# Performance work log

Measured on AMD Instinct MI355X. Metric: run time of the kernel, lower is better.

Reference implementation:

```python
import jax, jax.numpy as jnp
import numpy as np

N = 50000
NEG_SLOPE = 0.2


def add_self_loops(edge_index, n):
    loop = jnp.arange(n, dtype=edge_index.dtype)
    return jnp.concatenate([edge_index, jnp.stack([loop, loop])], axis=1)


def gatv2_conv(x, edge_index, Wl, bl, Wr, br, att, bias):
    """PyG GATv2Conv (share_weights=False, concat=True, add_self_loops applied by caller).
    x: [N, Fin]; edge_index: [2, E] with row0=src(j), row1=dst(i); att: [H, D].
    Returns (out [N, H*D], alpha [E, H])."""
    src, dst = edge_index[0], edge_index[1]
    H, D = att.shape
    n = x.shape[0]
    xl = (x @ Wl + bl).reshape(n, H, D)   # source-side transform
    xr = (x @ Wr + br).reshape(n, H, D)   # target-side transform
    e = jax.nn.leaky_relu(xl[src] + xr[dst], NEG_SLOPE)        # [E, H, D]
    logit = jnp.einsum('ehd,hd->eh', e, att)                    # [E, H]
    # segment softmax over edges grouped by target node
    lmax = jax.ops.segment_max(logit, dst, num_segments=n)      # [N, H]
    ex = jnp.exp(logit - lmax[dst])
    denom = jax.ops.segment_sum(ex, dst, num_segments=n)
    alpha = ex / denom[dst]                                     # [E, H]
    out = jax.ops.segment_sum(alpha[:, :, None] * xl[src], dst, num_segments=n)  # [N, H, D]
    return out.reshape(n, H * D) + bias, alpha


def setup_inputs() -> dict:
    key = jax.random.key(0)
    ks = jax.random.split(key, 16)
    E = 400000
    x = jax.random.normal(ks[0], (N, 23), dtype=jnp.float32)
    edge_index = jax.random.randint(ks[1], (2, E), 0, N, dtype=jnp.int64)
    H1, D1 = 8, 64
    F1 = H1 * D1  # 512
    s = 0.1
    return {
        'x': x,
        'edge_index': edge_index,
        'Wl1': jax.random.normal(ks[2], (23, F1), dtype=jnp.float32) * s,
        'bl1': jnp.zeros((F1,), jnp.float32),
        'Wr1': jax.random.normal(ks[3], (23, F1), dtype=jnp.float32) * s,
        'br1': jnp.zeros((F1,), jnp.float32),
        'att1': jax.random.normal(ks[4], (H1, D1), dtype=jnp.float32) * s,
        'bias1': jnp.zeros((F1,), jnp.float32),
        'Wl2': jax.random.normal(ks[5], (F1, 1), dtype=jnp.float32) * s,
        'bl2': jnp.zeros((1,), jnp.float32),
        'Wr2': jax.random.normal(ks[6], (F1, 1), dtype=jnp.float32) * s,
        'br2': jnp.zeros((1,), jnp.float32),
        'att2': jax.random.normal(ks[7], (1, 1), dtype=jnp.float32) * s,
        'bias2': jnp.zeros((1,), jnp.float32),
    }


def reference(x, edge_index, Wl1, bl1, Wr1, br1, att1, bias1,
              Wl2, bl2, Wr2, br2, att2, bias2):
    ei = add_self_loops(edge_index, N)
    h, _ = gatv2_conv(x, ei, Wl1, bl1, Wr1, br1, att1, bias1)
    h = jax.nn.relu(h)
    h, alpha = gatv2_conv(h, ei, Wl2, bl2, Wr2, br2, att2, bias2)
    return h, alpha
```

## Files before the change

### kernel.cpp

```cpp
#include <hip/hip_runtime.h>
#include <math.h>

#define NN 50000
#define E0 400000
#define EE 450000
#define FF 512
#define G1 2048
#define NPB 25
#define EPB 220
#define WAVES_TOTAL (G1 * 4)
#define MAXD 64
#define LOG2E 1.44269504f

typedef _Float16 h2 __attribute__((ext_vector_type(2)));

__device__ __forceinline__ h2 uas_h2(unsigned u) { union { unsigned u; h2 h; } c; c.u = u; return c.h; }
__device__ __forceinline__ unsigned h2as_u(h2 h) { union { unsigned u; h2 h; } c; c.h = h; return c.u; }
__device__ __forceinline__ float leaky(float v) { return fmaxf(v, 0.2f * v); }

__global__ __launch_bounds__(256) void k_predeg(
    const float* __restrict__ x,
    const float* __restrict__ Wl1, const float* __restrict__ bl1,
    const float* __restrict__ Wr1, const float* __restrict__ br1,
    const int* __restrict__ ei,
    unsigned* __restrict__ xlh, unsigned* __restrict__ xrh,
    int* __restrict__ cnt, uint2* __restrict__ slots)
{
    __shared__ float sx[NPB * 23];
    int b = blockIdx.x, t = threadIdx.x;

    {
        int e0 = b * EPB;
        int e1 = e0 + EPB; if (e1 > EE) e1 = EE;
        for (int e = e0 + t; e < e1; e += 256) {
            int src, dst;
            if (e < E0) { src = ei[e]; dst = ei[E0 + e]; }
            else        { src = e - E0; dst = src; }
            int p = atomicAdd(&cnt[dst], 1);
            if (p < MAXD) slots[(size_t)dst * MAXD + p] = make_uint2((unsigned)src, (unsigned)e);
        }
    }

    int i0 = b * NPB;
    int i1 = i0 + NPB; if (i1 > NN) i1 = NN;
    int nnod = i1 - i0;
    int nf = nnod * 23;
    for (int k = t; k < nf; k += 256) sx[k] = x[(size_t)i0 * 23 + k];
    __syncthreads();

    int c0 = 2 * t, c1 = 2 * t + 1;
    {
        float w0[23], w1[23];
#pragma unroll
        for (int r = 0; r < 23; r++) { w0[r] = Wl1[r * FF + c0]; w1[r] = Wl1[r * FF + c1]; }
        float bb0 = bl1[c0], bb1 = bl1[c1];
        for (int n = 0; n < nnod; n++) {
            float a0 = bb0, a1 = bb1;
#pragma unroll
            for (int r = 0; r < 23; r++) { float xv = sx[n * 23 + r]; a0 += xv * w0[r]; a1 += xv * w1[r]; }
            h2 hh = { (_Float16)a0, (_Float16)a1 };
            xlh[(size_t)(i0 + n) * 256 + t] = h2as_u(hh);
        }
    }
    {
        float w0[23], w1[23];
#pragma unroll
        for (int r = 0; r < 23; r++) { w0[r] = Wr1[r * FF + c0]; w1[r] = Wr1[r * FF + c1]; }
        float bb0 = br1[c0], bb1 = br1[c1];
        for (int n = 0; n < nnod; n++) {
            float a0 = bb0, a1 = bb1;
#pragma unroll
            for (int r = 0; r < 23; r++) { float xv = sx[n * 23 + r]; a0 += xv * w0[r]; a1 += xv * w1[r]; }
            h2 hh = { (_Float16)a0, (_Float16)a1 };
            xrh[(size_t)(i0 + n) * 256 + t] = h2as_u(hh);
        }
    }
}

__global__ __launch_bounds__(256) void k_layer1(
    const uint4* __restrict__ xlh, const uint4* __restrict__ xrh,
    const float* __restrict__ att, const float* __restrict__ bias1,
    const float* __restrict__ Wl2, const float* __restrict__ bl2,
    const float* __restrict__ Wr2, const float* __restrict__ br2,
    const int* __restrict__ cnt, const uint2* __restrict__ slots,
    float* __restrict__ xl2, float* __restrict__ xr2)
{
    int t = threadIdx.x;
    int l = t & 63;
    int wid = blockIdx.x * 4 + (t >> 6);

    float4 atA = ((const float4*)att)[2 * l];
    float4 atB = ((const float4*)att)[2 * l + 1];
    h2 a6_0 = { (_Float16)(0.6f * LOG2E * atA.x), (_Float16)(0.6f * LOG2E * atA.y) };
    h2 a6_1 = { (_Float16)(0.6f * LOG2E * atA.z), (_Float16)(0.6f * LOG2E * atA.w) };
    h2 a6_2 = { (_Float16)(0.6f * LOG2E * atB.x), (_Float16)(0.6f * LOG2E * atB.y) };
    h2 a6_3 = { (_Float16)(0.6f * LOG2E * atB.z), (_Float16)(0.6f * LOG2E * atB.w) };
    h2 a4_0 = { (_Float16)(0.4f * LOG2E * atA.x), (_Float16)(0.4f * LOG2E * atA.y) };
    h2 a4_1 = { (_Float16)(0.4f * LOG2E * atA.z), (_Float16)(0.4f * LOG2E * atA.w) };
    h2 a4_2 = { (_Float16)(0.4f * LOG2E * atB.x), (_Float16)(0.4f * LOG2E * atB.y) };
    h2 a4_3 = { (_Float16)(0.4f * LOG2E * atB.z), (_Float16)(0.4f * LOG2E * atB.w) };
    float bl2v = bl2[0], br2v = br2[0];

    for (int i = wid; i < NN; i += WAVES_TOTAL) {
        uint4 xq = xrh[(size_t)i * 64 + l];
        h2 q0 = uas_h2(xq.x), q1 = uas_h2(xq.y), q2 = uas_h2(xq.z), q3 = uas_h2(xq.w);

        float s = 0.f;
        h2 A0 = { 0, 0 }, A1 = { 0, 0 }, A2 = { 0, 0 }, A3 = { 0, 0 };

        int dg = cnt[i]; if (dg > MAXD) dg = MAXD;
        int myj = (l < dg) ? (int)slots[(size_t)i * MAXD + l].x : 0;

        int j0 = __builtin_amdgcn_readlane(myj, 0);
        uint4 r0 = xlh[(size_t)j0 * 64 + l];
        uint4 r1 = r0;
        if (dg > 1) r1 = xlh[(size_t)__builtin_amdgcn_readlane(myj, 1) * 64 + l];

        for (int p = 0; p < dg; p++) {
            uint4 rn = r0;
            if (p + 2 < dg)
                rn = xlh[(size_t)__builtin_amdgcn_readlane(myj, p + 2) * 64 + l];

            h2 p0 = uas_h2(r0.x), p1 = uas_h2(r0.y), p2 = uas_h2(r0.z), p3 = uas_h2(r0.w);
            h2 t0 = p0 + q0, t1 = p1 + q1, t2 = p2 + q2, t3 = p3 + q3;
            h2 b0 = uas_h2(h2as_u(t0) & 0x7fff7fffu);
            h2 b1 = uas_h2(h2as_u(t1) & 0x7fff7fffu);
            h2 b2 = uas_h2(h2as_u(t2) & 0x7fff7fffu);
            h2 b3 = uas_h2(h2as_u(t3) & 0x7fff7fffu);
            float part = 0.f;
            part = __builtin_amdgcn_fdot2(a6_0, t0, part, false);
            part = __builtin_amdgcn_fdot2(a4_0, b0, part, false);
            part = __builtin_amdgcn_fdot2(a6_1, t1, part, false);
            part = __builtin_amdgcn_fdot2(a4_1, b1, part, false);
            part = __builtin_amdgcn_fdot2(a6_2, t2, part, false);
            part = __builtin_amdgcn_fdot2(a4_2, b2, part, false);
            part = __builtin_amdgcn_fdot2(a6_3, t3, part, false);
            part = __builtin_amdgcn_fdot2(a4_3, b3, part, false);
            part += __shfl_xor(part, 1, 64);
            part += __shfl_xor(part, 2, 64);
            part += __shfl_xor(part, 4, 64);
            float wv = exp2f(part);
            s += wv;
            _Float16 wh = (_Float16)wv;
            h2 w2 = { wh, wh };
            A0 += w2 * p0;
            A1 += w2 * p1;
            A2 += w2 * p2;
            A3 += w2 * p3;
            r0 = r1; r1 = rn;
        }

        float inv = 1.f / s;
        float4 bA = ((const float4*)bias1)[2 * l];
        float4 bB = ((const float4*)bias1)[2 * l + 1];
        float h0 = fmaxf(fmaf((float)A0[0], inv, bA.x), 0.f);
        float h1 = fmaxf(fmaf((float)A0[1], inv, bA.y), 0.f);
        float h2v = fmaxf(fmaf((float)A1[0], inv, bA.z), 0.f);
        float h3 = fmaxf(fmaf((float)A1[1], inv, bA.w), 0.f);
        float h4 = fmaxf(fmaf((float)A2[0], inv, bB.x), 0.f);
        float h5 = fmaxf(fmaf((float)A2[1], inv, bB.y), 0.f);
        float h6 = fmaxf(fmaf((float)A3[0], inv, bB.z), 0.f);
        float h7 = fmaxf(fmaf((float)A3[1], inv, bB.w), 0.f);

        float4 wlA = ((const float4*)Wl2)[2 * l];
        float4 wlB = ((const float4*)Wl2)[2 * l + 1];
        float4 wrA = ((const float4*)Wr2)[2 * l];
        float4 wrB = ((const float4*)Wr2)[2 * l + 1];
        float pl = h0 * wlA.x + h1 * wlA.y + h2v * wlA.z + h3 * wlA.w
                 + h4 * wlB.x + h5 * wlB.y + h6 * wlB.z + h7 * wlB.w;
        float pr = h0 * wrA.x + h1 * wrA.y + h2v * wrA.z + h3 * wrA.w
                 + h4 * wrB.x + h5 * wrB.y + h6 * wrB.z + h7 * wrB.w;
#pragma unroll
        for (int o = 32; o > 0; o >>= 1) {
            pl += __shfl_xor(pl, o, 64);
            pr += __shfl_xor(pr, o, 64);
        }
        if (l == 0) {
            xl2[i] = pl + bl2v;
            xr2[i] = pr + br2v;
        }
    }
}

__global__ void k_layer2(const float* __restrict__ xl2, const float* __restrict__ xr2,
                         const float* __restrict__ att2, const float* __restrict__ bias2,
                         const int* __restrict__ cnt, const uint2* __restrict__ slots,
                         float* __restrict__ out)
{
    int i = blockIdx.x * blockDim.x + threadIdx.x;
    if (i >= NN) return;
    int dg = cnt[i]; if (dg > MAXD) dg = MAXD;
    const uint2* sl = slots + (size_t)i * MAXD;
    float xri = xr2[i];
    float a2l = att2[0] * LOG2E;
    float s = 0.f, num = 0.f;
    for (int p = 0; p < dg; p++) {
        float v = xl2[sl[p].x];
        float w = exp2f(leaky(v + xri) * a2l);
        s += w;
        num = fmaf(w, v, num);
    }
    out[i] = num / s + bias2[0];
    float inv = 1.f / s;
    for (int p = 0; p < dg; p++) {
        uint2 se = sl[p];
        float v = xl2[se.x];
        float w = exp2f(leaky(v + xri) * a2l);
        out[NN + se.y] = w * inv;
    }
}

extern "C" void kernel_launch(void* const* d_in, const int* in_sizes, int n_in,
                              void* d_out, int out_size, void* d_ws, size_t ws_size,
                              hipStream_t stream)
{
    const float* x     = (const float*)d_in[0];
    const int*   ei    = (const int*)d_in[1];
    const float* Wl1   = (const float*)d_in[2];
    const float* bl1   = (const float*)d_in[3];
    const float* Wr1   = (const float*)d_in[4];
    const float* br1   = (const float*)d_in[5];
    const float* att1  = (const float*)d_in[6];
    const float* bias1 = (const float*)d_in[7];
    const float* Wl2   = (const float*)d_in[8];
    const float* bl2   = (const float*)d_in[9];
    const float* Wr2   = (const float*)d_in[10];
    const float* br2   = (const float*)d_in[11];
    const float* att2  = (const float*)d_in[12];
    const float* bias2 = (const float*)d_in[13];
    float* out = (float*)d_out;

    char* ws = (char*)d_ws;
    unsigned* xlh  = (unsigned*)ws; ws += (size_t)NN * 256 * 4;
    unsigned* xrh  = (unsigned*)ws; ws += (size_t)NN * 256 * 4;
    float* xl2     = (float*)ws;    ws += (size_t)NN * 4;
    float* xr2     = (float*)ws;    ws += (size_t)NN * 4;
    int* cnt       = (int*)ws;      ws += (size_t)NN * 4;
    uint2* slots   = (uint2*)ws;    ws += (size_t)NN * MAXD * 8;

    hipMemsetAsync(cnt, 0, (size_t)NN * 4, stream);

    k_predeg<<<G1, 256, 0, stream>>>(x, Wl1, bl1, Wr1, br1, ei, xlh, xrh, cnt, slots);
    k_layer1<<<G1, 256, 0, stream>>>((const uint4*)xlh, (const uint4*)xrh,
                                     att1, bias1, Wl2, bl2, Wr2, br2,
                                     cnt, slots, xl2, xr2);
    k_layer2<<<(NN + 255) / 256, 256, 0, stream>>>(xl2, xr2, att2, bias2,
                                                   cnt, slots, out);
}
```

Measured before the change: 237.9 us.

## Use fp16 dot2 for first-layer projections and split edge slot arrays

The first-layer input projection now packs x rows and the Wl1/Wr1 weights into fp16 pairs and accumulates with fdot2 instructions, fusing the left and right transforms into a single pass over nodes. The interleaved (src, edge id) slot array becomes two separate int arrays, so layer 1 reads only the source indices. This cuts ALU work in the projection and the bytes fetched for neighbour lists. The cost is lower input precision (x and weights rounded to fp16) and an extra scattered store per edge when the slots are filled.

New measurement: 238.7 us. About the same (+0.3%).

```diff
diff --git a/kernel.cpp b/kernel.cpp
--- a/kernel.cpp
+++ b/kernel.cpp
@@ -16,6 +16,10 @@
 
 __device__ __forceinline__ h2 uas_h2(unsigned u) { union { unsigned u; h2 h; } c; c.u = u; return c.h; }
 __device__ __forceinline__ unsigned h2as_u(h2 h) { union { unsigned u; h2 h; } c; c.h = h; return c.u; }
+__device__ __forceinline__ unsigned packh(float a, float b) {
+    h2 hh = { (_Float16)a, (_Float16)b };
+    return h2as_u(hh);
+}
 __device__ __forceinline__ float leaky(float v) { return fmaxf(v, 0.2f * v); }
 
 __global__ __launch_bounds__(256) void k_predeg(
@@ -24,9 +28,9 @@
     const float* __restrict__ Wr1, const float* __restrict__ br1,
     const int* __restrict__ ei,
     unsigned* __restrict__ xlh, unsigned* __restrict__ xrh,
-    int* __restrict__ cnt, uint2* __restrict__ slots)
-{
-    __shared__ float sx[NPB * 23];
+    int* __restrict__ cnt, int* __restrict__ src_sl, int* __restrict__ eid_sl)
+{
+    __shared__ unsigned sxh[NPB * 12];
     int b = blockIdx.x, t = threadIdx.x;
 
     {
@@ -37,43 +41,61 @@
             if (e < E0) { src = ei[e]; dst = ei[E0 + e]; }
             else        { src = e - E0; dst = src; }
             int p = atomicAdd(&cnt[dst], 1);
-            if (p < MAXD) slots[(size_t)dst * MAXD + p] = make_uint2((unsigned)src, (unsigned)e);
+            if (p < MAXD) {
+                src_sl[(size_t)dst * MAXD + p] = src;
+                eid_sl[(size_t)dst * MAXD + p] = e;
+            }
         }
     }
 
     int i0 = b * NPB;
     int i1 = i0 + NPB; if (i1 > NN) i1 = NN;
     int nnod = i1 - i0;
-    int nf = nnod * 23;
-    for (int k = t; k < nf; k += 256) sx[k] = x[(size_t)i0 * 23 + k];
+    for (int k = t; k < nnod * 12; k += 256) {
+        int n = k / 12, j = k - n * 12;
+        const float* row = x + (size_t)(i0 + n) * 23;
+        float f0 = row[2 * j];
+        float f1 = (2 * j + 1 < 23) ? row[2 * j + 1] : 0.f;
+        sxh[n * 12 + j] = packh(f0, f1);
+    }
+
+    int c0 = 2 * t, c1 = 2 * t + 1;
+    h2 wl0[12], wl1[12], wr0[12], wr1[12];
+#pragma unroll
+    for (int j = 0; j < 12; j++) {
+        int r0 = 2 * j, r1 = 2 * j + 1;
+        float a, b2;
+        a = Wl1[r0 * FF + c0]; b2 = (r1 < 23) ? Wl1[r1 * FF + c0] : 0.f;
+        wl0[j] = (h2){ (_Float16)a, (_Float16)b2 };
+        a = Wl1[r0 * FF + c1]; b2 = (r1 < 23) ? Wl1[r1 * FF + c1] : 0.f;
+        wl1[j] = (h2){ (_Float16)a, (_Float16)b2 };
+        a = Wr1[r0 * FF + c0]; b2 = (r1 < 23) ? Wr1[r1 * FF + c0] : 0.f;
+        wr0[j] = (h2){ (_Float16)a, (_Float16)b2 };
+        a = Wr1[r0 * FF + c1]; b2 = (r1 < 23) ? Wr1[r1 * FF + c1] : 0.f;
+        wr1[j] = (h2){ (_Float16)a, (_Float16)b2 };
+    }
+    float bl0 = bl1[c0], bl1s = bl1[c1];
+    float br0 = br1[c0], br1s = br1[c1];
     __syncthreads();
 
-    int c0 = 2 * t, c1 = 2 * t + 1;
-    {
-        float w0[23], w1[23];
+    const uint4* S = (const uint4*)sxh;
+    for (int n = 0; n < nnod; n++) {
+        uint4 xa = S[n * 3 + 0];
+        uint4 xb = S[n * 3 + 1];
+        uint4 xc = S[n * 3 + 2];
+        h2 xv[12] = { uas_h2(xa.x), uas_h2(xa.y), uas_h2(xa.z), uas_h2(xa.w),
+                      uas_h2(xb.x), uas_h2(xb.y), uas_h2(xb.z), uas_h2(xb.w),
+                      uas_h2(xc.x), uas_h2(xc.y), uas_h2(xc.z), uas_h2(xc.w) };
+        float al0 = bl0, al1 = bl1s, ar0 = br0, ar1 = br1s;
 #pragma unroll
-        for (int r = 0; r < 23; r++) { w0[r] = Wl1[r * FF + c0]; w1[r] = Wl1[r * FF + c1]; }
-        float bb0 = bl1[c0], bb1 = bl1[c1];
-        for (int n = 0; n < nnod; n++) {
-            float a0 = bb0, a1 = bb1;
-#pragma unroll
-            for (int r = 0; r < 23; r++) { float xv = sx[n * 23 + r]; a0 += xv * w0[r]; a1 += xv * w1[r]; }
-            h2 hh = { (_Float16)a0, (_Float16)a1 };
-            xlh[(size_t)(i0 + n) * 256 + t] = h2as_u(hh);
-        }
-    }
-    {
-        float w0[23], w1[23];
-#pragma unroll
-        for (int r = 0; r < 23; r++) { w0[r] = Wr1[r * FF + c0]; w1[r] = Wr1[r * FF + c1]; }
-        float bb0 = br1[c0], bb1 = br1[c1];
-        for (int n = 0; n < nnod; n++) {
-            float a0 = bb0, a1 = bb1;
-#pragma unroll
-            for (int r = 0; r < 23; r++) { float xv = sx[n * 23 + r]; a0 += xv * w0[r]; a1 += xv * w1[r]; }
-            h2 hh = { (_Float16)a0, (_Float16)a1 };
-            xrh[(size_t)(i0 + n) * 256 + t] = h2as_u(hh);
-        }
+        for (int j = 0; j < 12; j++) {
+            al0 = __builtin_amdgcn_fdot2(wl0[j], xv[j], al0, false);
+            al1 = __builtin_amdgcn_fdot2(wl1[j], xv[j], al1, false);
+            ar0 = __builtin_amdgcn_fdot2(wr0[j], xv[j], ar0, false);
+            ar1 = __builtin_amdgcn_fdot2(wr1[j], xv[j], ar1, false);
+        }
+        xlh[(size_t)(i0 + n) * 256 + t] = packh(al0, al1);
+        xrh[(size_t)(i0 + n) * 256 + t] = packh(ar0, ar1);
     }
 }
 
@@ -82,7 +104,7 @@
     const float* __restrict__ att, const float* __restrict__ bias1,
     const float* __restrict__ Wl2, const float* __restrict__ bl2,
     const float* __restrict__ Wr2, const float* __restrict__ br2,
-    const int* __restrict__ cnt, const uint2* __restrict__ slots,
+    const int* __restrict__ cnt, const int* __restrict__ src_sl,
     float* __restrict__ xl2, float* __restrict__ xr2)
 {
     int t = threadIdx.x;
@@ -109,7 +131,7 @@
         h2 A0 = { 0, 0 }, A1 = { 0, 0 }, A2 = { 0, 0 }, A3 = { 0, 0 };
 
         int dg = cnt[i]; if (dg > MAXD) dg = MAXD;
-        int myj = (l < dg) ? (int)slots[(size_t)i * MAXD + l].x : 0;
+        int myj = (l < dg) ? src_sl[(size_t)i * MAXD + l] : 0;
 
         int j0 = __builtin_amdgcn_readlane(myj, 0);
         uint4 r0 = xlh[(size_t)j0 * 64 + l];
@@ -184,18 +206,19 @@
 
 __global__ void k_layer2(const float* __restrict__ xl2, const float* __restrict__ xr2,
                          const float* __restrict__ att2, const float* __restrict__ bias2,
-                         const int* __restrict__ cnt, const uint2* __restrict__ slots,
-                         float* __restrict__ out)
+                         const int* __restrict__ cnt, const int* __restrict__ src_sl,
+                         const int* __restrict__ eid_sl, float* __restrict__ out)
 {
     int i = blockIdx.x * blockDim.x + threadIdx.x;
     if (i >= NN) return;
     int dg = cnt[i]; if (dg > MAXD) dg = MAXD;
-    const uint2* sl = slots + (size_t)i * MAXD;
+    const int* sp = src_sl + (size_t)i * MAXD;
+    const int* ep = eid_sl + (size_t)i * MAXD;
     float xri = xr2[i];
     float a2l = att2[0] * LOG2E;
     float s = 0.f, num = 0.f;
     for (int p = 0; p < dg; p++) {
-        float v = xl2[sl[p].x];
+        float v = xl2[sp[p]];
         float w = exp2f(leaky(v + xri) * a2l);
         s += w;
         num = fmaf(w, v, num);
@@ -203,10 +226,9 @@
     out[i] = num / s + bias2[0];
     float inv = 1.f / s;
     for (int p = 0; p < dg; p++) {
-        uint2 se = sl[p];
-        float v = xl2[se.x];
+        float v = xl2[sp[p]];
         float w = exp2f(leaky(v + xri) * a2l);
-        out[NN + se.y] = w * inv;
+        out[NN + ep[p]] = w * inv;
     }
 }
 
@@ -236,14 +258,16 @@
     float* xl2     = (float*)ws;    ws += (size_t)NN * 4;
     float* xr2     = (float*)ws;    ws += (size_t)NN * 4;
     int* cnt       = (int*)ws;      ws += (size_t)NN * 4;
-    uint2* slots   = (uint2*)ws;    ws += (size_t)NN * MAXD * 8;
+    int* src_sl    = (int*)ws;      ws += (size_t)NN * MAXD * 4;
+    int* eid_sl    = (int*)ws;      ws += (size_t)NN * MAXD * 4;
 
     hipMemsetAsync(cnt, 0, (size_t)NN * 4, stream);
 
-    k_predeg<<<G1, 256, 0, stream>>>(x, Wl1, bl1, Wr1, br1, ei, xlh, xrh, cnt, slots);
+    k_predeg<<<G1, 256, 0, stream>>>(x, Wl1, bl1, Wr1, br1, ei, xlh, xrh,
+                                     cnt, src_sl, eid_sl);
     k_layer1<<<G1, 256, 0, stream>>>((const uint4*)xlh, (const uint4*)xrh,
                                      att1, bias1, Wl2, bl2, Wr2, br2,
-                                     cnt, slots, xl2, xr2);
+                                     cnt, src_sl, xl2, xr2);
     k_layer2<<<(NN + 255) / 256, 256, 0, stream>>>(xl2, xr2, att2, bias2,
-                                                   cnt, slots, out);
-}
+                                                   cnt, src_sl, eid_sl, out);
+}
```
